# Optimization experiments

Measured on AMD Instinct MI355X. Metric: run time of the kernel, lower is better.

Reference implementation:

```python
import jax, jax.numpy as jnp
import numpy as np

LUT_BITS = 4
IDX_PER_WORD = 32 // LUT_BITS  # 8 four-bit indices per int32 word
MASK = (1 << LUT_BITS) - 1


def setup_inputs() -> dict:
    key = jax.random.key(0)
    k1, k2, k3 = jax.random.split(key, 3)
    in_features, out_features, vec_sz = 8192, 8192, 2
    words_per_row = LUT_BITS * in_features // 32 // vec_sz  # 512
    inp = jax.random.normal(k1, (1, 16, in_features), dtype=jnp.float16)
    # packed codes: keep sign bit clear so arithmetic >> behaves as logical >>
    qweight = jax.random.randint(k2, (out_features, words_per_row), 0, 2147483647, dtype=jnp.int32)
    lut = jax.random.normal(k3, (1 << LUT_BITS, vec_sz), dtype=jnp.float16)
    return {"inp": inp, "qweight": qweight, "lut": lut}


def reference(inp, qweight, lut):
    O = qweight.shape[0]
    # unpack LUT_BITS-bit indices, little-endian within each int32 word
    shifts = (jnp.arange(IDX_PER_WORD, dtype=jnp.int32) * LUT_BITS)
    idx = (qweight[:, :, None] >> shifts[None, None, :]) & MASK  # (O, W, 8)
    idx = idx.reshape(O, -1)                                      # (O, in/vec_sz)
    # dequantize: each index selects a vec_sz vector from the LUT
    dq = lut[idx].reshape(O, -1)                                  # (O, in_features)
    x = inp.reshape(-1, dq.shape[1]).astype(dq.dtype)
    out = x @ dq.T                                                # (bs, O)
    return out.reshape(*inp.shape[:-1], O).astype(inp.dtype)
```

## Files before the change

kernel.cpp:

```cpp
#include <hip/hip_runtime.h>


typedef _Float16 half8 __attribute__((ext_vector_type(8)));
typedef _Float16 half4_t __attribute__((ext_vector_type(4)));
typedef float float4_t __attribute__((ext_vector_type(4)));

#define O_FEAT 8192
#define I_FEAT 8192
#define WAVES 16
#define K_PER_WAVE (I_FEAT / WAVES)
#define ITERS (K_PER_WAVE / 32)
#define TILES 2

__global__ void cvt_x_kernel(const float* __restrict__ x, _Float16* __restrict__ xf) {
    int i = (blockIdx.x * 256 + threadIdx.x) * 8;
    float4_t f0 = *(const float4_t*)(x + i);
    float4_t f1 = *(const float4_t*)(x + i + 4);
    half8 h = { (_Float16)f0[0], (_Float16)f0[1], (_Float16)f0[2], (_Float16)f0[3],
                (_Float16)f1[0], (_Float16)f1[1], (_Float16)f1[2], (_Float16)f1[3] };
    *(half8*)(xf + i) = h;
}

template <bool XF16>
__launch_bounds__(1024, 4)
__global__ void vq_gemm_kernel(const void* __restrict__ xsrc,
                               const unsigned short* __restrict__ qw,
                               const float* __restrict__ lutf,
                               float* __restrict__ out) {
    __shared__ half4_t pairlut[256];
    __shared__ float red[WAVES][TILES * 256];

    const int tid = threadIdx.x;
    if (tid < 256) {
        half4_t v;
        v[0] = (_Float16)lutf[(tid & 15) * 2 + 0];
        v[1] = (_Float16)lutf[(tid & 15) * 2 + 1];
        v[2] = (_Float16)lutf[(tid >> 4) * 2 + 0];
        v[3] = (_Float16)lutf[(tid >> 4) * 2 + 1];
        pairlut[tid] = v;
    }
    __syncthreads();

    const int wave = tid >> 6;
    const int lane = tid & 63;
    const int ln15 = lane & 15;
    const int kgrp = lane >> 4;

    const int obase = blockIdx.x * (TILES * 16);
    const int k0 = wave * K_PER_WAVE;

    const int xoff = ln15 * I_FEAT + k0 + kgrp * 8;
    const unsigned short* qp0 = qw + (obase + ln15) * 1024 + (k0 >> 3) + kgrp;
    const unsigned short* qp1 = qp0 + 16 * 1024;

    float4_t acc0 = {0.f, 0.f, 0.f, 0.f};
    float4_t acc1 = {0.f, 0.f, 0.f, 0.f};

#pragma unroll 4
    for (int it = 0; it < ITERS; ++it) {
        half8 a;
        if constexpr (XF16) {
            a = *(const half8*)((const _Float16*)xsrc + xoff + it * 32);
        } else {
            const float* xp = (const float*)xsrc + xoff + it * 32;
            float4_t f0 = *(const float4_t*)xp;
            float4_t f1 = *(const float4_t*)(xp + 4);
            a = (half8){ (_Float16)f0[0], (_Float16)f0[1], (_Float16)f0[2], (_Float16)f0[3],
                         (_Float16)f1[0], (_Float16)f1[1], (_Float16)f1[2], (_Float16)f1[3] };
        }
        unsigned int q0 = qp0[it * 4];
        unsigned int q1 = qp1[it * 4];
        half4_t p00 = pairlut[q0 & 0xFF];
        half4_t p01 = pairlut[(q0 >> 8) & 0xFF];
        half4_t p10 = pairlut[q1 & 0xFF];
        half4_t p11 = pairlut[(q1 >> 8) & 0xFF];
        half8 b0 = __builtin_shufflevector(p00, p01, 0, 1, 2, 3, 4, 5, 6, 7);
        half8 b1 = __builtin_shufflevector(p10, p11, 0, 1, 2, 3, 4, 5, 6, 7);
        acc0 = __builtin_amdgcn_mfma_f32_16x16x32_f16(a, b0, acc0, 0, 0, 0);
        acc1 = __builtin_amdgcn_mfma_f32_16x16x32_f16(a, b1, acc1, 0, 0, 0);
    }

#pragma unroll
    for (int r = 0; r < 4; ++r) {
        red[wave][0 * 256 + (kgrp * 4 + r) * 16 + ln15] = acc0[r];
        red[wave][1 * 256 + (kgrp * 4 + r) * 16 + ln15] = acc1[r];
    }
    __syncthreads();

    if (tid < TILES * 256) {
        float s = 0.f;
#pragma unroll
        for (int w = 0; w < WAVES; ++w)
            s += red[w][tid];
        const int t = tid >> 8;
        const int m = (tid >> 4) & 15;
        const int n = tid & 15;
        out[m * O_FEAT + obase + t * 16 + n] = s;
    }
}

extern "C" void kernel_launch(void* const* d_in, const int* in_sizes, int n_in,
                              void* d_out, int out_size, void* d_ws, size_t ws_size,
                              hipStream_t stream) {
    const float* x = (const float*)d_in[0];
    const unsigned short* qw = (const unsigned short*)d_in[1];
    const float* lutf = (const float*)d_in[2];
    float* out = (float*)d_out;

    dim3 grid(O_FEAT / (TILES * 16));
    dim3 block(1024);

    if (ws_size >= (size_t)(16 * I_FEAT * 2)) {
        cvt_x_kernel<<<dim3(16 * I_FEAT / (256 * 8)), dim3(256), 0, stream>>>(x, (_Float16*)d_ws);
        vq_gemm_kernel<true><<<grid, block, 0, stream>>>(d_ws, qw, lutf, out);
    } else {
        vq_gemm_kernel<false><<<grid, block, 0, stream>>>(x, qw, lutf, out);
    }
}
```

Measured before the change: 88.37 us.

## Preload packed weights with wide vector loads and remap K per lane group

Each lane group now owns a contiguous 128-element K slice and loads its 32 bytes of packed weight codes per tile up front, as two 16-byte vector loads. This replaces the per-iteration strided 2-byte loads. The x loads are remapped to the same K slice, so the MFMA reduction stays correct. The weight loads are issued before the barrier that waits for the LUT build, so the two can overlap. The cross-wave reduction now writes float4 accumulators directly. The cost is higher register pressure from holding the codes and a fully unrolled loop.

```diff
diff --git a/kernel.cpp b/kernel.cpp
--- a/kernel.cpp
+++ b/kernel.cpp
@@ -4,12 +4,13 @@
 typedef _Float16 half8 __attribute__((ext_vector_type(8)));
 typedef _Float16 half4_t __attribute__((ext_vector_type(4)));
 typedef float float4_t __attribute__((ext_vector_type(4)));
+typedef unsigned int uint4_t __attribute__((ext_vector_type(4)));
 
 #define O_FEAT 8192
 #define I_FEAT 8192
 #define WAVES 16
 #define K_PER_WAVE (I_FEAT / WAVES)
-#define ITERS (K_PER_WAVE / 32)
+#define NJ (K_PER_WAVE / 32)
 #define TILES 2
 
 __global__ void cvt_x_kernel(const float* __restrict__ x, _Float16* __restrict__ xf) {
@@ -24,11 +25,11 @@
 template <bool XF16>
 __launch_bounds__(1024, 4)
 __global__ void vq_gemm_kernel(const void* __restrict__ xsrc,
-                               const unsigned short* __restrict__ qw,
+                               const unsigned char* __restrict__ qwb,
                                const float* __restrict__ lutf,
                                float* __restrict__ out) {
     __shared__ half4_t pairlut[256];
-    __shared__ float red[WAVES][TILES * 256];
+    __shared__ float4_t red[WAVES][TILES * 64];
 
     const int tid = threadIdx.x;
     if (tid < 256) {
@@ -39,63 +40,70 @@
         v[3] = (_Float16)lutf[(tid >> 4) * 2 + 1];
         pairlut[tid] = v;
     }
-    __syncthreads();
 
     const int wave = tid >> 6;
     const int lane = tid & 63;
     const int ln15 = lane & 15;
-    const int kgrp = lane >> 4;
+    const int g    = lane >> 4;
 
     const int obase = blockIdx.x * (TILES * 16);
-    const int k0 = wave * K_PER_WAVE;
 
-    const int xoff = ln15 * I_FEAT + k0 + kgrp * 8;
-    const unsigned short* qp0 = qw + (obase + ln15) * 1024 + (k0 >> 3) + kgrp;
-    const unsigned short* qp1 = qp0 + 16 * 1024;
+    const unsigned char* qp0 = qwb + (size_t)(obase + ln15) * 2048 + wave * 128 + g * 32;
+    const unsigned char* qp1 = qp0 + 16 * 2048;
+
+    uint4_t qa0 = *(const uint4_t*)(qp0);
+    uint4_t qb0 = *(const uint4_t*)(qp0 + 16);
+    uint4_t qa1 = *(const uint4_t*)(qp1);
+    uint4_t qb1 = *(const uint4_t*)(qp1 + 16);
+
+    const int xoff = ln15 * I_FEAT + wave * K_PER_WAVE + 128 * g;
+
+    __syncthreads();
 
     float4_t acc0 = {0.f, 0.f, 0.f, 0.f};
     float4_t acc1 = {0.f, 0.f, 0.f, 0.f};
 
-#pragma unroll 4
-    for (int it = 0; it < ITERS; ++it) {
+#pragma unroll
+    for (int j = 0; j < NJ; ++j) {
         half8 a;
         if constexpr (XF16) {
-            a = *(const half8*)((const _Float16*)xsrc + xoff + it * 32);
+            a = *(const half8*)((const _Float16*)xsrc + xoff + 8 * j);
         } else {
-            const float* xp = (const float*)xsrc + xoff + it * 32;
+            const float* xp = (const float*)xsrc + xoff + 8 * j;
             float4_t f0 = *(const float4_t*)xp;
             float4_t f1 = *(const float4_t*)(xp + 4);
             a = (half8){ (_Float16)f0[0], (_Float16)f0[1], (_Float16)f0[2], (_Float16)f0[3],
                          (_Float16)f1[0], (_Float16)f1[1], (_Float16)f1[2], (_Float16)f1[3] };
         }
-        unsigned int q0 = qp0[it * 4];
-        unsigned int q1 = qp1[it * 4];
-        half4_t p00 = pairlut[q0 & 0xFF];
-        half4_t p01 = pairlut[(q0 >> 8) & 0xFF];
-        half4_t p10 = pairlut[q1 & 0xFF];
-        half4_t p11 = pairlut[(q1 >> 8) & 0xFF];
+        unsigned int w0 = (j < 8) ? qa0[(j >> 1) & 3] : qb0[(j >> 1) & 3];
+        unsigned int w1 = (j < 8) ? qa1[(j >> 1) & 3] : qb1[(j >> 1) & 3];
+        if (j & 1) { w0 >>= 16; w1 >>= 16; }
+        half4_t p00 = pairlut[w0 & 0xFF];
+        half4_t p01 = pairlut[(w0 >> 8) & 0xFF];
+        half4_t p10 = pairlut[w1 & 0xFF];
+        half4_t p11 = pairlut[(w1 >> 8) & 0xFF];
         half8 b0 = __builtin_shufflevector(p00, p01, 0, 1, 2, 3, 4, 5, 6, 7);
         half8 b1 = __builtin_shufflevector(p10, p11, 0, 1, 2, 3, 4, 5, 6, 7);
         acc0 = __builtin_amdgcn_mfma_f32_16x16x32_f16(a, b0, acc0, 0, 0, 0);
         acc1 = __builtin_amdgcn_mfma_f32_16x16x32_f16(a, b1, acc1, 0, 0, 0);
     }
 
-#pragma unroll
-    for (int r = 0; r < 4; ++r) {
-        red[wave][0 * 256 + (kgrp * 4 + r) * 16 + ln15] = acc0[r];
-        red[wave][1 * 256 + (kgrp * 4 + r) * 16 + ln15] = acc1[r];
-    }
+    red[wave][lane] = acc0;
+    red[wave][64 + lane] = acc1;
     __syncthreads();
 
-    if (tid < TILES * 256) {
+    if (tid < 512) {
+        const float* rf = (const float*)red;
         float s = 0.f;
 #pragma unroll
         for (int w = 0; w < WAVES; ++w)
-            s += red[w][tid];
-        const int t = tid >> 8;
-        const int m = (tid >> 4) & 15;
-        const int n = tid & 15;
-        out[m * O_FEAT + obase + t * 16 + n] = s;
+            s += rf[w * (TILES * 64 * 4) + tid];
+        const int t2 = tid >> 8;
+        const int l  = (tid >> 2) & 63;
+        const int r  = tid & 3;
+        const int m  = (l >> 4) * 4 + r;
+        const int n  = l & 15;
+        out[m * O_FEAT + obase + t2 * 16 + n] = s;
     }
 }
 
@@ -103,7 +111,7 @@
                               void* d_out, int out_size, void* d_ws, size_t ws_size,
                               hipStream_t stream) {
     const float* x = (const float*)d_in[0];
-    const unsigned short* qw = (const unsigned short*)d_in[1];
+    const unsigned char* qwb = (const unsigned char*)d_in[1];
     const float* lutf = (const float*)d_in[2];
     float* out = (float*)d_out;
 
@@ -112,8 +120,8 @@
 
     if (ws_size >= (size_t)(16 * I_FEAT * 2)) {
         cvt_x_kernel<<<dim3(16 * I_FEAT / (256 * 8)), dim3(256), 0, stream>>>(x, (_Float16*)d_ws);
-        vq_gemm_kernel<true><<<grid, block, 0, stream>>>(d_ws, qw, lutf, out);
+        vq_gemm_kernel<true><<<grid, block, 0, stream>>>(d_ws, qwb, lutf, out);
     } else {
-        vq_gemm_kernel<false><<<grid, block, 0, stream>>>(x, qw, lutf, out);
+        vq_gemm_kernel<false><<<grid, block, 0, stream>>>(x, qwb, lutf, out);
     }
 }
```

Measured after the change: 81.08 us. 8.3% less time.
